# Kernel optimization log

Hardware: AMD Instinct MI355X
Metric: run time of the kernel (lower is better)

## Reference

```python
import jax, jax.numpy as jnp
import numpy as np

A_CONST = 0.1
B_CONST = 0.2
C_CONST = 0.8

INPUT_SIZE = 1024
HIDDEN_SIZE = 2048
BATCH = 32768
SIGMA = 0.02


def acti_func(x, a, b, c):
    # piecewise: a*(1 - x/b) for x<=b ; 0 for b<x<c ; a*(x-c)/(1-c) for x>=c
    low = -a * x / b + a
    high = a * x / (1.0 - c) + a * c / (c - 1.0)
    return jnp.where(x <= b, low, jnp.where(x >= c, high, jnp.zeros_like(x)))


def setup_inputs() -> dict:
    key = jax.random.key(0)
    ks = jax.random.split(key, 4)
    x = jax.random.normal(ks[0], (BATCH, INPUT_SIZE), dtype=jnp.float32)
    W0 = jax.random.normal(ks[1], (INPUT_SIZE, HIDDEN_SIZE), dtype=jnp.float32) * SIGMA
    b0 = jnp.zeros((HIDDEN_SIZE,), dtype=jnp.float32)
    W1 = jax.random.normal(ks[2], (HIDDEN_SIZE, HIDDEN_SIZE), dtype=jnp.float32) * SIGMA
    b1 = jnp.zeros((HIDDEN_SIZE,), dtype=jnp.float32)
    W2 = jax.random.normal(ks[3], (HIDDEN_SIZE, 1), dtype=jnp.float32) * SIGMA
    b2 = jnp.zeros((1,), dtype=jnp.float32)
    return {"x": x, "W0": W0, "b0": b0, "W1": W1, "b1": b1, "W2": W2, "b2": b2}


def reference(x, W0, b0, W1, b1, W2, b2):
    h = jax.nn.elu(x @ W0 + b0)
    h = jax.nn.elu(h @ W1 + b1)
    out = jax.nn.sigmoid(h @ W2 + b2)  # [B, 1]
    alpha = acti_func(out, A_CONST, B_CONST, C_CONST)
    return out, alpha
```

## Files before the change

kernel.cpp:

```cpp
#include <hip/hip_runtime.h>
#include <hip/hip_bf16.h>
#include <stdint.h>

typedef unsigned short u16;
typedef __bf16 bf16x8 __attribute__((ext_vector_type(8)));
typedef float floatx4 __attribute__((ext_vector_type(4)));

__device__ __forceinline__ u16 f2bf(float f) {
  union { float f; unsigned u; } c; c.f = f;
  unsigned r = c.u + 0x7fffu + ((c.u >> 16) & 1u);
  return (u16)(r >> 16);
}

__device__ __forceinline__ void load_lds16(const void* g, void* l) {
  __builtin_amdgcn_global_load_lds(
      (const __attribute__((address_space(1))) void*)g,
      (__attribute__((address_space(3))) void*)l,
      16, 0, 0);
}

__device__ __forceinline__ void memclob() { asm volatile("" ::: "memory"); }
__device__ __forceinline__ void barrier_() {
  memclob();
  __builtin_amdgcn_s_barrier();
  memclob();
}

__global__ __launch_bounds__(256) void preamble(
    const float* __restrict__ x, const float* __restrict__ W0,
    const float* __restrict__ W1,
    u16* __restrict__ Xb, u16* __restrict__ Wt0, u16* __restrict__ Wt1,
    float* __restrict__ z)
{
  __shared__ float tile[32][33];
  const int bid = blockIdx.x;
  const int t = threadIdx.x;

  if (bid < 32768) {
    int i = bid * 256 + t;
    float4 f = ((const float4*)x)[i];
    ushort4 u;
    u.x = f2bf(f.x); u.y = f2bf(f.y); u.z = f2bf(f.z); u.w = f2bf(f.w);
    ((ushort4*)Xb)[i] = u;
  } else if (bid < 32768 + 2048) {
    int tb = bid - 32768;
    int bx = (tb & 63) * 32, by = (tb >> 6) * 32;
    int tx = t & 31, ty = t >> 5;
    #pragma unroll
    for (int i = 0; i < 32; i += 8)
      tile[ty + i][tx] = W0[(size_t)(by + ty + i) * 2048 + bx + tx];
    __syncthreads();
    #pragma unroll
    for (int i = 0; i < 32; i += 8)
      Wt0[(size_t)(bx + ty + i) * 1024 + by + tx] = f2bf(tile[tx][ty + i]);
  } else if (bid < 32768 + 2048 + 4096) {
    int tb = bid - (32768 + 2048);
    int bx = (tb & 63) * 32, by = (tb >> 6) * 32;
    int tx = t & 31, ty = t >> 5;
    #pragma unroll
    for (int i = 0; i < 32; i += 8)
      tile[ty + i][tx] = W1[(size_t)(by + ty + i) * 2048 + bx + tx];
    __syncthreads();
    #pragma unroll
    for (int i = 0; i < 32; i += 8)
      Wt1[(size_t)(bx + ty + i) * 2048 + by + tx] = f2bf(tile[tx][ty + i]);
  } else {
    int tb = bid - (32768 + 2048 + 4096);
    ((float4*)z)[tb * 256 + t] = (float4){0.f, 0.f, 0.f, 0.f};
  }
}

template<bool FUSE_HEAD, int KK>
__global__ __launch_bounds__(512, 2) void gemm256_8p(
    const u16* __restrict__ A,
    const u16* __restrict__ Bt,
    const float* __restrict__ bias,
    u16* __restrict__ C,
    const float* __restrict__ W2,
    float* __restrict__ z,
    int M, int N)
{
  __shared__ u16 lds[65536];

  const int t = threadIdx.x;
  const int l = t & 63;
  const int w = t >> 6;
  const int wm = w >> 2;
  const int wn = w & 3;
  const int lm = l & 15;
  const int q  = l >> 4;

  const int nwg = gridDim.x;
  int wg = blockIdx.x;
  wg = (wg & 7) * (nwg >> 3) + (wg >> 3);
  const int nbn = N >> 8;
  const int n0 = (wg % nbn) << 8;
  const int m0 = (wg / nbn) << 8;

  const int rowoff = t >> 3;
  const int lc8 = ((t & 7) ^ (rowoff & 7)) * 8;
  const int bq = rowoff >> 5;
  const int br = rowoff & 31;
  const u16* rA0 = A  + (size_t)(m0 + rowoff) * KK + lc8;
  const u16* rA1 = A  + (size_t)(m0 + 128 + rowoff) * KK + lc8;
  const u16* rB0 = Bt + (size_t)(n0 + bq * 64 + br) * KK + lc8;
  const u16* rB1 = Bt + (size_t)(n0 + (2 + bq) * 64 + br) * KK + lc8;
  const int ldst = t * 8;

#define SLOT(p, idx) (((p) * 4 + (idx)) * 8192)

#define STG_A(P, S, KOFF) do {                                                 \
    load_lds16(rA0 + (S) * 64 * KK + (KOFF), &lds[SLOT(P, S) + ldst]);         \
    load_lds16(rA1 + (S) * 64 * KK + (KOFF), &lds[SLOT(P, S) + 4096 + ldst]);  \
  } while (0)
#define STG_B(P, S, KOFF) do {                                                 \
    load_lds16(rB0 + (S) * 32 * KK + (KOFF), &lds[SLOT(P, 2 + (S)) + ldst]);   \
    load_lds16(rB1 + (S) * 32 * KK + (KOFF), &lds[SLOT(P, 2 + (S)) + 4096 + ldst]); \
  } while (0)

  const int ck0 = ((0 * 4 + q) ^ (lm & 7)) * 8;
  const int ck1 = ((1 * 4 + q) ^ (lm & 7)) * 8;
  const int arow = (wm * 64 + lm) * 64;
  const int brow = (wn * 32 + lm) * 64;
#define RDA(p, i, ck) (*(const bf16x8*)&lds[SLOT(p, (i) >> 2) + arow + ((i) & 3) * 1024 + (ck)])
#define RDB(p, j, ck) (*(const bf16x8*)&lds[SLOT(p, 2 + ((j) >> 1)) + brow + ((j) & 1) * 1024 + (ck)])
#define MFMA(d, x, y) d = __builtin_amdgcn_mfma_f32_16x16x32_bf16(x, y, d, 0, 0, 0)

  floatx4 acc[8][4];
  #pragma unroll
  for (int i = 0; i < 8; ++i)
    #pragma unroll
    for (int j = 0; j < 4; ++j)
      acc[i][j] = (floatx4){0.f, 0.f, 0.f, 0.f};

  bf16x8 a[8][2];
  bf16x8 b[2][2];

  constexpr int NK = KK >> 6;
  static_assert(NK >= 4 && (NK & 1) == 0, "NK must be even, >= 4");

#define VMW6 asm volatile("s_waitcnt vmcnt(6)" ::: "memory")
#define VMW0 asm volatile("s_waitcnt vmcnt(0)" ::: "memory")
#define VMWN do {} while (0)

#define KTILE(P, SB1, OB1, SN2, ON2, VMW)                                      \
  {                                                                            \
    _Pragma("unroll")                                                          \
    for (int i = 0; i < 4; ++i) { a[i][0] = RDA(P, i, ck0); a[i][1] = RDA(P, i, ck1); } \
    _Pragma("unroll")                                                          \
    for (int j = 0; j < 2; ++j) { b[j][0] = RDB(P, j, ck0); b[j][1] = RDB(P, j, ck1); } \
    if (SB1) { STG_B((P) ^ 1, 1, OB1); }                                       \
    barrier_();                                                                \
    __builtin_amdgcn_s_setprio(1);                                             \
    _Pragma("unroll")                                                          \
    for (int i = 0; i < 4; ++i)                                                \
      _Pragma("unroll")                                                        \
      for (int j = 0; j < 2; ++j) {                                            \
        MFMA(acc[i][j], a[i][0], b[j][0]);                                     \
        MFMA(acc[i][j], a[i][1], b[j][1]);                                     \
      }                                                                        \
    __builtin_amdgcn_s_setprio(0);                                             \
    barrier_();                                                                \
    _Pragma("unroll")                                                          \
    for (int i = 4; i < 8; ++i) { a[i][0] = RDA(P, i, ck0); a[i][1] = RDA(P, i, ck1); } \
    if (SN2) { STG_A(P, 0, ON2); }                                             \
    barrier_();                                                                \
    __builtin_amdgcn_s_setprio(1);                                             \
    _Pragma("unroll")                                                          \
    for (int i = 4; i < 8; ++i)                                                \
      _Pragma("unroll")                                                        \
      for (int j = 0; j < 2; ++j) {                                            \
        MFMA(acc[i][j], a[i][0], b[j][0]);                                     \
        MFMA(acc[i][j], a[i][1], b[j][1]);                                     \
      }                                                                        \
    __builtin_amdgcn_s_setprio(0);                                             \
    barrier_();                                                                \
    _Pragma("unroll")                                                          \
    for (int j = 0; j < 2; ++j) { b[j][0] = RDB(P, 2 + j, ck0); b[j][1] = RDB(P, 2 + j, ck1); } \
    if (SN2) { STG_A(P, 1, ON2); }                                             \
    barrier_();                                                                \
    __builtin_amdgcn_s_setprio(1);                                             \
    _Pragma("unroll")                                                          \
    for (int i = 0; i < 4; ++i)                                                \
      _Pragma("unroll")                                                        \
      for (int j = 0; j < 2; ++j) {                                            \
        MFMA(acc[i][2 + j], a[i][0], b[j][0]);                                 \
        MFMA(acc[i][2 + j], a[i][1], b[j][1]);                                 \
      }                                                                        \
    __builtin_amdgcn_s_setprio(0);                                             \
    barrier_();                                                                \
    if (SN2) { STG_B(P, 0, ON2); }                                             \
    VMW;                                                                       \
    barrier_();                                                                \
    __builtin_amdgcn_s_setprio(1);                                             \
    _Pragma("unroll")                                                          \
    for (int i = 4; i < 8; ++i)                                                \
      _Pragma("unroll")                                                        \
      for (int j = 0; j < 2; ++j) {                                            \
        MFMA(acc[i][2 + j], a[i][0], b[j][0]);                                 \
        MFMA(acc[i][2 + j], a[i][1], b[j][1]);                                 \
      }                                                                        \
    __builtin_amdgcn_s_setprio(0);                                             \
    barrier_();                                                                \
  }

  STG_A(0, 0, 0); memclob(); STG_A(0, 1, 0); memclob();
  STG_B(0, 0, 0); memclob(); STG_B(0, 1, 0); memclob();
  STG_A(1, 0, 64); memclob(); STG_A(1, 1, 64); memclob();
  STG_B(1, 0, 64);
  VMW6;
  barrier_();

  #pragma unroll 1
  for (int g = 0; g < NK - 2; g += 2) {
    KTILE(0, true, 64, true, 128, VMW6);
    KTILE(1, true, 128, true, 192, VMW6);
    rA0 += 128; rA1 += 128; rB0 += 128; rB1 += 128;
  }
  KTILE(0, true, 64, false, 0, VMW0);
  KTILE(1, false, 0, false, 0, VMWN);

  float bv[4];
  #pragma unroll
  for (int j = 0; j < 4; ++j) bv[j] = bias[n0 + wn * 64 + j * 16 + lm];

  if (!FUSE_HEAD) {
    #pragma unroll
    for (int i = 0; i < 8; ++i) {
      #pragma unroll
      for (int r = 0; r < 4; ++r) {
        int grow = m0 + wm * 128 + i * 16 + q * 4 + r;
        size_t base = (size_t)grow * N + n0 + wn * 64 + lm;
        #pragma unroll
        for (int j = 0; j < 4; ++j) {
          float v = acc[i][j][r] + bv[j];
          v = v > 0.f ? v : (__expf(v) - 1.f);
          C[base + j * 16] = f2bf(v);
        }
      }
    }
  } else {
    float w2v[4];
    #pragma unroll
    for (int j = 0; j < 4; ++j) w2v[j] = W2[n0 + wn * 64 + j * 16 + lm];
    #pragma unroll
    for (int i = 0; i < 8; ++i) {
      #pragma unroll
      for (int r = 0; r < 4; ++r) {
        float pacc = 0.f;
        #pragma unroll
        for (int j = 0; j < 4; ++j) {
          float v = acc[i][j][r] + bv[j];
          v = v > 0.f ? v : (__expf(v) - 1.f);
          pacc += v * w2v[j];
        }
        pacc += __shfl_xor(pacc, 1);
        pacc += __shfl_xor(pacc, 2);
        pacc += __shfl_xor(pacc, 4);
        pacc += __shfl_xor(pacc, 8);
        if (lm == 0) atomicAdd(&z[m0 + wm * 128 + i * 16 + q * 4 + r], pacc);
      }
    }
  }
#undef SLOT
#undef STG_A
#undef STG_B
#undef RDA
#undef RDB
#undef MFMA
#undef KTILE
#undef VMW6
#undef VMW0
#undef VMWN
}

__global__ __launch_bounds__(256) void sigmoid_alpha(
    const float* __restrict__ z, const float* __restrict__ b2,
    float* __restrict__ out, int B)
{
  int i = blockIdx.x * blockDim.x + threadIdx.x;
  if (i >= B) return;
  float o = 1.f / (1.f + expf(-(z[i] + b2[0])));
  float alpha;
  if (o <= 0.2f)      alpha = 0.1f - 0.5f * o;
  else if (o >= 0.8f) alpha = 0.5f * o - 0.4f;
  else                alpha = 0.f;
  out[i] = o;
  out[B + i] = alpha;
}

extern "C" void kernel_launch(void* const* d_in, const int* in_sizes, int n_in,
                              void* d_out, int out_size, void* d_ws, size_t ws_size,
                              hipStream_t stream) {
  const int BATCH = 32768, HID = 2048;

  const float* x  = (const float*)d_in[0];
  const float* W0 = (const float*)d_in[1];
  const float* b0 = (const float*)d_in[2];
  const float* W1 = (const float*)d_in[3];
  const float* b1 = (const float*)d_in[4];
  const float* W2 = (const float*)d_in[5];
  const float* b2 = (const float*)d_in[6];
  float* out = (float*)d_out;

  char* ws = (char*)d_ws;
  u16* Xb   = (u16*)(ws);
  u16* Wt0  = (u16*)(ws + (size_t)67108864);
  u16* Wt1  = (u16*)(ws + (size_t)71303168);
  u16* h0   = (u16*)(ws + (size_t)79691776);
  float* z  = (float*)(ws + (size_t)213909504);

  const int grid = (BATCH / 256) * (HID / 256);

  preamble<<<32768 + 2048 + 4096 + 32, 256, 0, stream>>>(x, W0, W1, Xb, Wt0, Wt1, z);
  gemm256_8p<false, 1024><<<grid, 512, 0, stream>>>(
      Xb, Wt0, b0, h0, nullptr, nullptr, BATCH, HID);
  gemm256_8p<true, 2048><<<grid, 512, 0, stream>>>(
      h0, Wt1, b1, nullptr, W2, z, BATCH, HID);
  sigmoid_alpha<<<BATCH / 256, 256, 0, stream>>>(z, b2, out, BATCH);
}
```

Measured before the change: 692.8 us.

## Restructure GEMM k-tile into four-phase schedule with fewer barriers

Reorganises the per-k-tile schedule of the bf16 MFMA GEMM from eight barrier-separated phases to four. Both A sub-tiles are kept in separate register sets (a0, a1) so they are loaded once and reused across both B halves. Global-to-LDS staging is regrouped, and absolute k offsets replace the pointer increments. This cuts barrier count per tile and overlaps LDS reads with MFMA issue, at the cost of more live registers and less separation between LDS writes and reads, which could hurt occupancy or correctness.

```diff
diff --git a/kernel.cpp b/kernel.cpp
--- a/kernel.cpp
+++ b/kernel.cpp
@@ -71,7 +71,7 @@
 }
 
 template<bool FUSE_HEAD, int KK>
-__global__ __launch_bounds__(512, 2) void gemm256_8p(
+__global__ __launch_bounds__(512, 2) void gemm256_p4(
     const u16* __restrict__ A,
     const u16* __restrict__ Bt,
     const float* __restrict__ bias,
@@ -133,8 +133,9 @@
     for (int j = 0; j < 4; ++j)
       acc[i][j] = (floatx4){0.f, 0.f, 0.f, 0.f};
 
-  bf16x8 a[8][2];
-  bf16x8 b[2][2];
+  bf16x8 a0[4][2];
+  bf16x8 a1[4][2];
+  bf16x8 bb[2][2];
 
   constexpr int NK = KK >> 6;
   static_assert(NK >= 4 && (NK & 1) == 0, "NK must be even, >= 4");
@@ -143,65 +144,64 @@
 #define VMW0 asm volatile("s_waitcnt vmcnt(0)" ::: "memory")
 #define VMWN do {} while (0)
 
-#define KTILE(P, SB1, OB1, SN2, ON2, VMW)                                      \
+#define KTILE(P, S1, KO1, S2, KO2, VMW)                                        \
   {                                                                            \
-    _Pragma("unroll")                                                          \
-    for (int i = 0; i < 4; ++i) { a[i][0] = RDA(P, i, ck0); a[i][1] = RDA(P, i, ck1); } \
-    _Pragma("unroll")                                                          \
-    for (int j = 0; j < 2; ++j) { b[j][0] = RDB(P, j, ck0); b[j][1] = RDB(P, j, ck1); } \
-    if (SB1) { STG_B((P) ^ 1, 1, OB1); }                                       \
+           \
+    _Pragma("unroll")                                                          \
+    for (int i = 0; i < 4; ++i) { a0[i][0] = RDA(P, i, ck0); a0[i][1] = RDA(P, i, ck1); } \
+    _Pragma("unroll")                                                          \
+    for (int j = 0; j < 2; ++j) { bb[j][0] = RDB(P, j, ck0); bb[j][1] = RDB(P, j, ck1); } \
+    if (S1) { STG_B((P) ^ 1, 1, KO1); }                                        \
     barrier_();                                                                \
     __builtin_amdgcn_s_setprio(1);                                             \
     _Pragma("unroll")                                                          \
     for (int i = 0; i < 4; ++i)                                                \
       _Pragma("unroll")                                                        \
       for (int j = 0; j < 2; ++j) {                                            \
-        MFMA(acc[i][j], a[i][0], b[j][0]);                                     \
-        MFMA(acc[i][j], a[i][1], b[j][1]);                                     \
+        MFMA(acc[i][j], a0[i][0], bb[j][0]);                                   \
+        MFMA(acc[i][j], a0[i][1], bb[j][1]);                                   \
       }                                                                        \
     __builtin_amdgcn_s_setprio(0);                                             \
-    barrier_();                                                                \
-    _Pragma("unroll")                                                          \
-    for (int i = 4; i < 8; ++i) { a[i][0] = RDA(P, i, ck0); a[i][1] = RDA(P, i, ck1); } \
-    if (SN2) { STG_A(P, 0, ON2); }                                             \
-    barrier_();                                                                \
-    __builtin_amdgcn_s_setprio(1);                                             \
-    _Pragma("unroll")                                                          \
-    for (int i = 4; i < 8; ++i)                                                \
-      _Pragma("unroll")                                                        \
-      for (int j = 0; j < 2; ++j) {                                            \
-        MFMA(acc[i][j], a[i][0], b[j][0]);                                     \
-        MFMA(acc[i][j], a[i][1], b[j][1]);                                     \
-      }                                                                        \
-    __builtin_amdgcn_s_setprio(0);                                             \
-    barrier_();                                                                \
-    _Pragma("unroll")                                                          \
-    for (int j = 0; j < 2; ++j) { b[j][0] = RDB(P, 2 + j, ck0); b[j][1] = RDB(P, 2 + j, ck1); } \
-    if (SN2) { STG_A(P, 1, ON2); }                                             \
+                                   \
+    _Pragma("unroll")                                                          \
+    for (int i = 0; i < 4; ++i) { a1[i][0] = RDA(P, 4 + i, ck0); a1[i][1] = RDA(P, 4 + i, ck1); } \
     barrier_();                                                                \
     __builtin_amdgcn_s_setprio(1);                                             \
     _Pragma("unroll")                                                          \
     for (int i = 0; i < 4; ++i)                                                \
       _Pragma("unroll")                                                        \
       for (int j = 0; j < 2; ++j) {                                            \
-        MFMA(acc[i][2 + j], a[i][0], b[j][0]);                                 \
-        MFMA(acc[i][2 + j], a[i][1], b[j][1]);                                 \
+        MFMA(acc[4 + i][j], a1[i][0], bb[j][0]);                               \
+        MFMA(acc[4 + i][j], a1[i][1], bb[j][1]);                               \
       }                                                                        \
     __builtin_amdgcn_s_setprio(0);                                             \
+      \
+    _Pragma("unroll")                                                          \
+    for (int j = 0; j < 2; ++j) { bb[j][0] = RDB(P, 2 + j, ck0); bb[j][1] = RDB(P, 2 + j, ck1); } \
+    if (S2) { STG_A(P, 0, KO2); }                                              \
     barrier_();                                                                \
-    if (SN2) { STG_B(P, 0, ON2); }                                             \
+    __builtin_amdgcn_s_setprio(1);                                             \
+    _Pragma("unroll")                                                          \
+    for (int i = 0; i < 4; ++i)                                                \
+      _Pragma("unroll")                                                        \
+      for (int j = 0; j < 2; ++j) {                                            \
+        MFMA(acc[i][2 + j], a0[i][0], bb[j][0]);                               \
+        MFMA(acc[i][2 + j], a0[i][1], bb[j][1]);                               \
+      }                                                                        \
+    __builtin_amdgcn_s_setprio(0);                                             \
+           \
+    if (S2) { STG_A(P, 1, KO2); STG_B(P, 0, KO2); }                            \
     VMW;                                                                       \
     barrier_();                                                                \
     __builtin_amdgcn_s_setprio(1);                                             \
     _Pragma("unroll")                                                          \
-    for (int i = 4; i < 8; ++i)                                                \
+    for (int i = 0; i < 4; ++i)                                                \
       _Pragma("unroll")                                                        \
       for (int j = 0; j < 2; ++j) {                                            \
-        MFMA(acc[i][2 + j], a[i][0], b[j][0]);                                 \
-        MFMA(acc[i][2 + j], a[i][1], b[j][1]);                                 \
+        MFMA(acc[4 + i][2 + j], a1[i][0], bb[j][0]);                           \
+        MFMA(acc[4 + i][2 + j], a1[i][1], bb[j][1]);                           \
       }                                                                        \
     __builtin_amdgcn_s_setprio(0);                                             \
-    barrier_();                                                                \
   }
 
   STG_A(0, 0, 0); memclob(); STG_A(0, 1, 0); memclob();
@@ -213,11 +213,11 @@
 
   #pragma unroll 1
   for (int g = 0; g < NK - 2; g += 2) {
-    KTILE(0, true, 64, true, 128, VMW6);
-    KTILE(1, true, 128, true, 192, VMW6);
-    rA0 += 128; rA1 += 128; rB0 += 128; rB1 += 128;
+    const int k1 = (g + 1) * 64, k2 = (g + 2) * 64, k3 = (g + 3) * 64;
+    KTILE(0, true, k1, true, k2, VMW6);
+    KTILE(1, true, k2, true, k3, VMW6);
   }
-  KTILE(0, true, 64, false, 0, VMW0);
+  KTILE(0, true, (NK - 1) * 64, false, 0, VMW0);
   KTILE(1, false, 0, false, 0, VMWN);
 
   float bv[4];
@@ -313,9 +313,9 @@
   const int grid = (BATCH / 256) * (HID / 256);
 
   preamble<<<32768 + 2048 + 4096 + 32, 256, 0, stream>>>(x, W0, W1, Xb, Wt0, Wt1, z);
-  gemm256_8p<false, 1024><<<grid, 512, 0, stream>>>(
+  gemm256_p4<false, 1024><<<grid, 512, 0, stream>>>(
       Xb, Wt0, b0, h0, nullptr, nullptr, BATCH, HID);
-  gemm256_8p<true, 2048><<<grid, 512, 0, stream>>>(
+  gemm256_p4<true, 2048><<<grid, 512, 0, stream>>>(
       h0, Wt1, b1, nullptr, W2, z, BATCH, HID);
   sigmoid_alpha<<<BATCH / 256, 256, 0, stream>>>(z, b2, out, BATCH);
 }
```

Result: faster. 643.7 us (-7.1%).
